# Kernel tuning notes

Hardware: AMD Instinct MI355X
Metric: run time of the kernel (lower is better)

Reference implementation:

```python
import jax, jax.numpy as jnp
import numpy as np

N_NODES = 100000
N_EDGES = 1600000
IN_FEATS = 128
HIDDEN = 128


def _graph_conv(x, W, b, src, dst, n_nodes):
    # DGL GraphConv with norm='both': out = D_in^{-1/2} * A^T * (D_out^{-1/2} * x) @ W + b
    ones = jnp.ones((src.shape[0],), dtype=x.dtype)
    deg_out = jax.ops.segment_sum(ones, src, num_segments=n_nodes)
    deg_in = jax.ops.segment_sum(ones, dst, num_segments=n_nodes)
    norm_src = jax.lax.rsqrt(jnp.clip(deg_out, 1.0))  # [N]
    norm_dst = jax.lax.rsqrt(jnp.clip(deg_in, 1.0))   # [N]
    h = x @ W                                          # [N, F_out]
    msg = h[src] * norm_src[src][:, None]              # gather by edge src: [E, F_out]
    agg = jax.ops.segment_sum(msg, dst, num_segments=n_nodes)  # scatter-add to dst
    return agg * norm_dst[:, None] + b


def setup_inputs() -> dict:
    key = jax.random.key(0)
    ks = jax.random.split(key, 9)
    x = jax.random.normal(ks[0], (N_NODES, IN_FEATS), dtype=jnp.float32)
    src = jax.random.randint(ks[1], (N_EDGES,), 0, N_NODES, dtype=jnp.int32)
    dst = jax.random.randint(ks[2], (N_EDGES,), 0, N_NODES, dtype=jnp.int32)
    s1 = 1.0 / np.sqrt(IN_FEATS)
    s2 = 1.0 / np.sqrt(HIDDEN)
    W1 = jax.random.uniform(ks[3], (IN_FEATS, HIDDEN), jnp.float32, -s1, s1)
    b1 = jnp.zeros((HIDDEN,), jnp.float32)
    W2 = jax.random.uniform(ks[4], (HIDDEN, HIDDEN), jnp.float32, -s2, s2)
    b2 = jnp.zeros((HIDDEN,), jnp.float32)
    sp = 1.0 / np.sqrt(2 * HIDDEN)
    Wp = jax.random.uniform(ks[5], (2 * HIDDEN, 1), jnp.float32, -sp, sp)
    bp = jax.random.uniform(ks[6], (1,), jnp.float32, -sp, sp)
    return {"x": x, "W1": W1, "b1": b1, "W2": W2, "b2": b2,
            "Wp": Wp, "bp": bp, "src": src, "dst": dst}


def reference(x, W1, b1, W2, b2, Wp, bp, src, dst):
    n_nodes = x.shape[0]
    h = _graph_conv(x, W1, b1, src, dst, n_nodes)
    h = jax.nn.relu(h)
    h = _graph_conv(h, W2, b2, src, dst, n_nodes)  # final node embeddings [N, H]
    # predict_links on the same edge list: cat(h[u], h[v]) -> linear -> sigmoid
    edge_h = jnp.concatenate([h[src], h[dst]], axis=1)  # [E, 2H]
    scores = jax.nn.sigmoid(edge_h @ Wp + bp)           # [E, 1]
    return scores
```

## Files before the change

### kernel.cpp

```cpp
#include <hip/hip_runtime.h>
#include <cstdint>
#include <cstddef>

#define NN 100000
#define NE 1600000
#define F  128
#define NPAD 100352
#define NBUCK 782
#define BCAPG 2560
#define FILLB 384
#define CHUNK 4167

typedef __attribute__((ext_vector_type(8))) short bf16x8;
typedef __attribute__((ext_vector_type(4))) float f32x4;

__device__ __forceinline__ unsigned short f2bf(float f) {
    unsigned u = __float_as_uint(f);
    unsigned r = (u + 0x7fffu + ((u >> 16) & 1u)) >> 16;
    return (unsigned short)r;
}
__device__ __forceinline__ void acc_bf8s(const uint4 v, const float ns, float* acc) {
    acc[0] += __uint_as_float(v.x << 16) * ns;
    acc[1] += __uint_as_float(v.x & 0xffff0000u) * ns;
    acc[2] += __uint_as_float(v.y << 16) * ns;
    acc[3] += __uint_as_float(v.y & 0xffff0000u) * ns;
    acc[4] += __uint_as_float(v.z << 16) * ns;
    acc[5] += __uint_as_float(v.z & 0xffff0000u) * ns;
    acc[6] += __uint_as_float(v.w << 16) * ns;
    acc[7] += __uint_as_float(v.w & 0xffff0000u) * ns;
}

__global__ void head_const_kernel(const float* __restrict__ b2, const float* __restrict__ Wp,
                                  const float* __restrict__ bp, float* __restrict__ consts) {
    const int l = threadIdx.x;
    const float2 bb = *(const float2*)&b2[2 * l];
    const float2 wa = *(const float2*)&Wp[2 * l];
    const float2 wc = *(const float2*)&Wp[F + 2 * l];
    float s = bb.x * (wa.x + wc.x) + bb.y * (wa.y + wc.y);
    #pragma unroll
    for (int m = 32; m > 0; m >>= 1) s += __shfl_xor(s, m);
    if (l == 0) consts[0] = s + bp[0];
}

__global__ void headw_kernel(const float* __restrict__ W2, const float* __restrict__ Wp,
                             float2* __restrict__ V) {
    const int i = threadIdx.x;
    float sa = 0.f, sc = 0.f;
    #pragma unroll 8
    for (int j = 0; j < F; ++j) {
        const float w = W2[i * F + j];
        sa += w * Wp[j];
        sc += w * Wp[F + j];
    }
    V[i] = make_float2(sa, sc);
}

__global__ void init_cursor_kernel(int* __restrict__ gCur) {
    const int b = blockIdx.x * blockDim.x + threadIdx.x;
    if (b < NBUCK) gCur[b] = b * BCAPG;
}

__global__ __launch_bounds__(256, 3)
void gemm1_fill_kernel(const float* __restrict__ in, const float* __restrict__ W,
                       unsigned short* __restrict__ out_bf,
                       const int* __restrict__ src, const int* __restrict__ dst,
                       int* __restrict__ deg_out, int* __restrict__ gCur,
                       int* __restrict__ srcPart) {
    __shared__ __align__(16) char smem[31264];

    const int g = blockIdx.x;
    const int tid = threadIdx.x;

    if (g & 1) {
        int* packedL = (int*)smem;
        unsigned short* bktL = (unsigned short*)(packedL + CHUNK);
        int* hist = (int*)((char*)smem + 25008);
        int* curL = hist + NBUCK;
        const int e0 = (g >> 1) * CHUNK;
        const int nCh = min(CHUNK, NE - e0);
        for (int i = tid; i < NBUCK; i += 256) hist[i] = 0;
        __syncthreads();
        for (int i = tid; i < nCh; i += 256) {
            const int s = src[e0 + i];
            const int d = dst[e0 + i];
            atomicAdd(&deg_out[s], 1);
            const int bkt = d >> 7;
            atomicAdd(&hist[bkt], 1);
            packedL[i] = s | ((d & 127) << 17);
            bktL[i] = (unsigned short)bkt;
        }
        __syncthreads();
        for (int b = tid; b < NBUCK; b += 256) {
            const int c = hist[b];
            curL[b] = (c > 0) ? atomicAdd(&gCur[b], c) : 0;
        }
        __syncthreads();
        for (int i = tid; i < nCh; i += 256) {
            const int bkt = bktL[i];
            const int p = atomicAdd(&curL[bkt], 1);
            if (p < (bkt + 1) * BCAPG)
                srcPart[p] = packedL[i];
        }
        return;
    }

    char* A_hi = smem;
    char* A_lo = smem + 8192;

    const int gid  = g >> 1;
    const int w    = tid >> 6;
    const int lane = tid & 63;
    const int ml   = lane & 15;
    const int quad = lane >> 4;

    bf16x8 Bf[4][2];
    #pragma unroll
    for (int kb = 0; kb < 4; ++kb) {
        #pragma unroll
        for (int nb = 0; nb < 2; ++nb) {
            const int n = 32 * w + nb * 16 + ml;
            const int k0 = kb * 32 + quad * 8;
            #pragma unroll
            for (int j = 0; j < 8; ++j)
                Bf[kb][nb][j] = (short)f2bf(W[(k0 + j) * F + n]);
        }
    }

    const int nTiles = NN / 32;
    for (int tile = gid; tile < nTiles; tile += 384) {
        const int row0 = tile * 32;
        __syncthreads();
        #pragma unroll
        for (int c = 0; c < 2; ++c) {
            const int i2 = tid + 256 * c;
            const int m  = i2 >> 4;
            const int o  = i2 & 15;
            const float* xr = &in[(size_t)(row0 + m) * F + o * 8];
            const float4 v0 = *(const float4*)xr;
            const float4 v1 = *(const float4*)(xr + 4);
            float xv[8] = {v0.x, v0.y, v0.z, v0.w, v1.x, v1.y, v1.z, v1.w};
            short hi8[8], lo8[8];
            #pragma unroll
            for (int j = 0; j < 8; ++j) {
                const unsigned short h = f2bf(xv[j]);
                hi8[j] = (short)h;
                lo8[j] = (short)f2bf(xv[j] - __uint_as_float((unsigned)h << 16));
            }
            const int kb2 = o >> 2, q2 = o & 3, ml2 = m & 15, mh2 = m >> 4;
            const int fo = (((mh2 * 4 + kb2) * 64) + q2 * 16 + ml2) * 16;
            *(bf16x8*)(A_hi + fo) = *(bf16x8*)hi8;
            *(bf16x8*)(A_lo + fo) = *(bf16x8*)lo8;
        }
        __syncthreads();

        f32x4 acc00 = {0,0,0,0}, acc01 = {0,0,0,0}, acc10 = {0,0,0,0}, acc11 = {0,0,0,0};
        #pragma unroll
        for (int kb = 0; kb < 4; ++kb) {
            const int o0 = (kb * 64 + lane) * 16;
            const int o1 = ((4 + kb) * 64 + lane) * 16;
            const bf16x8 ah0 = *(const bf16x8*)(A_hi + o0);
            const bf16x8 ah1 = *(const bf16x8*)(A_hi + o1);
            const bf16x8 al0 = *(const bf16x8*)(A_lo + o0);
            const bf16x8 al1 = *(const bf16x8*)(A_lo + o1);
            acc00 = __builtin_amdgcn_mfma_f32_16x16x32_bf16(ah0, Bf[kb][0], acc00, 0, 0, 0);
            acc00 = __builtin_amdgcn_mfma_f32_16x16x32_bf16(al0, Bf[kb][0], acc00, 0, 0, 0);
            acc01 = __builtin_amdgcn_mfma_f32_16x16x32_bf16(ah0, Bf[kb][1], acc01, 0, 0, 0);
            acc01 = __builtin_amdgcn_mfma_f32_16x16x32_bf16(al0, Bf[kb][1], acc01, 0, 0, 0);
            acc10 = __builtin_amdgcn_mfma_f32_16x16x32_bf16(ah1, Bf[kb][0], acc10, 0, 0, 0);
            acc10 = __builtin_amdgcn_mfma_f32_16x16x32_bf16(al1, Bf[kb][0], acc10, 0, 0, 0);
            acc11 = __builtin_amdgcn_mfma_f32_16x16x32_bf16(ah1, Bf[kb][1], acc11, 0, 0, 0);
            acc11 = __builtin_amdgcn_mfma_f32_16x16x32_bf16(al1, Bf[kb][1], acc11, 0, 0, 0);
        }

        #pragma unroll
        for (int mh = 0; mh < 2; ++mh) {
            #pragma unroll
            for (int nb = 0; nb < 2; ++nb) {
                const f32x4 a = (mh == 0) ? (nb == 0 ? acc00 : acc01)
                                          : (nb == 0 ? acc10 : acc11);
                const int row = row0 + mh * 16 + quad * 4;
                const int col = 32 * w + nb * 16 + ml;
                #pragma unroll
                for (int r = 0; r < 4; ++r)
                    out_bf[(size_t)(row + r) * F + col] = f2bf(a[r]);
            }
        }
    }
}

__global__ void normsrc_kernel(const int* __restrict__ deg_out, float* __restrict__ norm_src, int nN) {
    const int n = blockIdx.x * blockDim.x + threadIdx.x;
    if (n < nN) norm_src[n] = rsqrtf((float)max(deg_out[n], 1));
}

__global__ __launch_bounds__(256)
void gather_sort_kernel(const unsigned short* __restrict__ hs,
                        int* __restrict__ srcPart, const int* __restrict__ gCur,
                        const float* __restrict__ norm_src, const float* __restrict__ bias,
                        const float2* __restrict__ V, float2* __restrict__ uw,
                        int* __restrict__ offs, int* __restrict__ ends,
                        float* __restrict__ norm_dst) {
    __shared__ int cnt[128];
    __shared__ int loc[128];
    __shared__ int cur[128];
    __shared__ int sortedL[BCAPG];

    const int b   = blockIdx.x;
    const int tid = threadIdx.x;
    const int nlo = b * 128;
    const int nCnt = min(128, NN - nlo);
    const int eBase = b * BCAPG;
    const int total = min(gCur[b] - eBase, BCAPG);

    if (tid < 128) cnt[tid] = 0;
    __syncthreads();
    for (int i = tid; i < total; i += 256)
        atomicAdd(&cnt[(srcPart[eBase + i] >> 17) & 127], 1);
    __syncthreads();
    if (tid < 128) loc[tid] = cnt[tid];
    __syncthreads();
    for (int off = 1; off < 128; off <<= 1) {
        int v = 0;
        if (tid < 128 && tid >= off) v = loc[tid - off];
        __syncthreads();
        if (tid < 128) loc[tid] += v;
        __syncthreads();
    }
    if (tid < 128) cur[tid] = loc[tid] - cnt[tid];
    if (tid < nCnt) {
        const int st = eBase + loc[tid] - cnt[tid];
        offs[nlo + tid] = st;
        ends[nlo + tid] = st + cnt[tid];
        norm_dst[nlo + tid] = rsqrtf((float)max(cnt[tid], 1));
    }
    __syncthreads();
    for (int i = tid; i < total; i += 256) {
        const int v = srcPart[eBase + i];
        const int r = atomicAdd(&cur[(v >> 17) & 127], 1);
        sortedL[r] = v & 0x1FFFF;
    }
    __syncthreads();
    for (int i = tid; i < total; i += 256)
        srcPart[eBase + i] = sortedL[i];

    const int w  = tid >> 6;
    const int l  = tid & 63;
    const int q  = l >> 4;
    const int c8 = (l & 15) * 8;
    float bb[8];
    *(float4*)&bb[0] = *(const float4*)&bias[c8];
    *(float4*)&bb[4] = *(const float4*)&bias[c8 + 4];
    float2 Vl[8];
    #pragma unroll
    for (int k = 0; k < 8; ++k) Vl[k] = V[c8 + k];

    const int nhEnd = min((w + 1) * 32, nCnt);
    for (int nh = w * 32; nh < nhEnd; ++nh) {
        const int end = loc[nh];
        const int beg = end - cnt[nh];
        float acc[8] = {0.f, 0.f, 0.f, 0.f, 0.f, 0.f, 0.f, 0.f};
        int j = beg;
        for (; j + 16 <= end; j += 16) {
            const int s0 = sortedL[j + q];
            const int s1 = sortedL[j + 4 + q];
            const int s2 = sortedL[j + 8 + q];
            const int s3 = sortedL[j + 12 + q];
            const float ns0 = norm_src[s0];
            const float ns1 = norm_src[s1];
            const float ns2 = norm_src[s2];
            const float ns3 = norm_src[s3];
            const uint4 v0 = *(const uint4*)&hs[(size_t)s0 * F + c8];
            const uint4 v1 = *(const uint4*)&hs[(size_t)s1 * F + c8];
            const uint4 v2 = *(const uint4*)&hs[(size_t)s2 * F + c8];
            const uint4 v3 = *(const uint4*)&hs[(size_t)s3 * F + c8];
            acc_bf8s(v0, ns0, acc);
            acc_bf8s(v1, ns1, acc);
            acc_bf8s(v2, ns2, acc);
            acc_bf8s(v3, ns3, acc);
        }
        for (; j + 8 <= end; j += 8) {
            const int s0 = sortedL[j + q];
            const int s1 = sortedL[j + 4 + q];
            const float ns0 = norm_src[s0];
            const float ns1 = norm_src[s1];
            const uint4 v0 = *(const uint4*)&hs[(size_t)s0 * F + c8];
            const uint4 v1 = *(const uint4*)&hs[(size_t)s1 * F + c8];
            acc_bf8s(v0, ns0, acc);
            acc_bf8s(v1, ns1, acc);
        }
        for (; j + 4 <= end; j += 4) {
            const int s = sortedL[j + q];
            const float ns = norm_src[s];
            const uint4 v = *(const uint4*)&hs[(size_t)s * F + c8];
            acc_bf8s(v, ns, acc);
        }
        if (j + q < end) {
            const int s = sortedL[j + q];
            const float ns = norm_src[s];
            const uint4 v = *(const uint4*)&hs[(size_t)s * F + c8];
            acc_bf8s(v, ns, acc);
        }
        #pragma unroll
        for (int k = 0; k < 8; ++k) {
            acc[k] += __shfl_xor(acc[k], 16);
            acc[k] += __shfl_xor(acc[k], 32);
        }

        const int n = nlo + nh;
        const float nd = rsqrtf((float)max(cnt[nh], 1));
        float pa = 0.f, pc = 0.f;
        #pragma unroll
        for (int k = 0; k < 8; ++k) {
            const float ok = fmaxf(acc[k] * nd + bb[k], 0.f);
            pa += ok * Vl[k].x;
            pc += ok * Vl[k].y;
        }
        #pragma unroll
        for (int m = 1; m <= 8; m <<= 1) {
            pa += __shfl_xor(pa, m);
            pc += __shfl_xor(pc, m);
        }
        if (l == 0) {
            const float ns = norm_src[n];
            uw[n] = make_float2(ns * pa, ns * pc);
        }
    }
}

__global__ void ac_kernel(const float2* __restrict__ uw, const int* __restrict__ sorted_src,
                          const int* __restrict__ offs, const int* __restrict__ ends,
                          const float* __restrict__ norm_dst,
                          float* __restrict__ A, float* __restrict__ C, int nN) {
    const int n = blockIdx.x * blockDim.x + threadIdx.x;
    if (n >= nN) return;
    const int beg = offs[n];
    const int end = ends[n];
    float su = 0.f, sw = 0.f;
    int j = beg;
    for (; j + 2 <= end; j += 2) {
        const float2 t0 = uw[sorted_src[j]];
        const float2 t1 = uw[sorted_src[j + 1]];
        su += t0.x + t1.x;
        sw += t0.y + t1.y;
    }
    if (j < end) {
        const float2 t = uw[sorted_src[j]];
        su += t.x;
        sw += t.y;
    }
    const float nd = norm_dst[n];
    A[n] = nd * su;
    C[n] = nd * sw;
}

__global__ void score_kernel(const float* __restrict__ A, const float* __restrict__ C,
                             const int* __restrict__ src, const int* __restrict__ dst,
                             const float* __restrict__ consts, float* __restrict__ out, int nE) {
    const int e = blockIdx.x * blockDim.x + threadIdx.x;
    if (e < nE) {
        const float z = A[src[e]] + C[dst[e]] + consts[0];
        out[e] = 1.f / (1.f + __expf(-z));
    }
}

extern "C" void kernel_launch(void* const* d_in, const int* in_sizes, int n_in,
                              void* d_out, int out_size, void* d_ws, size_t ws_size,
                              hipStream_t stream) {
    const float* x  = (const float*)d_in[0];
    const float* W1 = (const float*)d_in[1];
    const float* b1 = (const float*)d_in[2];
    const float* W2 = (const float*)d_in[3];
    const float* b2 = (const float*)d_in[4];
    const float* Wp = (const float*)d_in[5];
    const float* bp = (const float*)d_in[6];
    const int*   src = (const int*)d_in[7];
    const int*   dst = (const int*)d_in[8];
    float* out = (float*)d_out;

    float* ws        = (float*)d_ws;
    float* norm_src  = ws;
    float* bufA      = ws + NPAD;
    float* bufC      = ws + 2 * NPAD;
    float* norm_dst  = ws + 3 * NPAD;
    int*   offs      = (int*)(ws + 4 * NPAD);
    int*   ends      = offs + NPAD;
    int*   gCur      = ends + NPAD;
    float* consts    = (float*)(gCur + 1024);
    float2* V        = (float2*)(consts + 16);
    float2* uw       = V + 128;
    int*   srcPart   = (int*)(uw + NN);
    unsigned short* hs_bf = (unsigned short*)(srcPart + NBUCK * BCAPG);

    hipMemsetAsync(bufA, 0, NPAD * sizeof(int), stream);
    init_cursor_kernel<<<4, 256, 0, stream>>>(gCur);
    head_const_kernel<<<1, 64, 0, stream>>>(b2, Wp, bp, consts);
    headw_kernel<<<1, 128, 0, stream>>>(W2, Wp, V);

    gemm1_fill_kernel<<<768, 256, 0, stream>>>(x, W1, hs_bf, src, dst,
                                               (int*)bufA, gCur, srcPart);

    normsrc_kernel<<<(NN + 255) / 256, 256, 0, stream>>>((const int*)bufA, norm_src, NN);

    gather_sort_kernel<<<NBUCK, 256, 0, stream>>>(hs_bf, srcPart, gCur, norm_src, b1,
                                                  V, uw, offs, ends, norm_dst);

    ac_kernel<<<(NN + 255) / 256, 256, 0, stream>>>(uw, srcPart, offs, ends, norm_dst,
                                                    bufA, bufC, NN);

    score_kernel<<<(NE + 255) / 256, 256, 0, stream>>>(bufA, bufC, src, dst, consts, out, NE);
}
```

Baseline: 314.8 us.

## Split hidden features into column quarters and gather per quarter to improve cache reuse

The GEMM now writes the bf16 hidden matrix as four column-quarter planes of 32 features each. A separate gather kernel runs one pass per quarter, and a combine kernel sums the four partial head projections. The sort kernel writes sorted indices to a new buffer, and extra blocks pre-scale the hidden rows by norm_src in place so the gather skips the per-edge norm load. Each quarter plane is about 6.4MB, which should fit better in cache during the random gathers. The cost is more kernel launches, an extra read-modify-write pass over the hidden matrix, a second bf16 rounding after scaling, and re-reading the sorted indices four times.

```diff
diff --git a/kernel.cpp b/kernel.cpp
--- a/kernel.cpp
+++ b/kernel.cpp
@@ -8,8 +8,8 @@
 #define NPAD 100352
 #define NBUCK 782
 #define BCAPG 2560
-#define FILLB 384
 #define CHUNK 4167
+#define SCALEB 512
 
 typedef __attribute__((ext_vector_type(8))) short bf16x8;
 typedef __attribute__((ext_vector_type(4))) float f32x4;
@@ -19,15 +19,16 @@
     unsigned r = (u + 0x7fffu + ((u >> 16) & 1u)) >> 16;
     return (unsigned short)r;
 }
-__device__ __forceinline__ void acc_bf8s(const uint4 v, const float ns, float* acc) {
-    acc[0] += __uint_as_float(v.x << 16) * ns;
-    acc[1] += __uint_as_float(v.x & 0xffff0000u) * ns;
-    acc[2] += __uint_as_float(v.y << 16) * ns;
-    acc[3] += __uint_as_float(v.y & 0xffff0000u) * ns;
-    acc[4] += __uint_as_float(v.z << 16) * ns;
-    acc[5] += __uint_as_float(v.z & 0xffff0000u) * ns;
-    acc[6] += __uint_as_float(v.w << 16) * ns;
-    acc[7] += __uint_as_float(v.w & 0xffff0000u) * ns;
+__device__ __forceinline__ void acc_bf4(const uint2 v, float* acc) {
+    acc[0] += __uint_as_float(v.x << 16);
+    acc[1] += __uint_as_float(v.x & 0xffff0000u);
+    acc[2] += __uint_as_float(v.y << 16);
+    acc[3] += __uint_as_float(v.y & 0xffff0000u);
+}
+__device__ __forceinline__ unsigned scale2bf(unsigned p, float ns) {
+    const float a = __uint_as_float(p << 16) * ns;
+    const float b = __uint_as_float(p & 0xffff0000u) * ns;
+    return (unsigned)f2bf(a) | ((unsigned)f2bf(b) << 16);
 }
 
 __global__ void head_const_kernel(const float* __restrict__ b2, const float* __restrict__ Wp,
@@ -125,6 +126,8 @@
                 Bf[kb][nb][j] = (short)f2bf(W[(k0 + j) * F + n]);
         }
     }
+
+    unsigned short* outq = out_bf + (size_t)w * NN * 32;
 
     const int nTiles = NN / 32;
     for (int tile = gid; tile < nTiles; tile += 384) {
@@ -179,10 +182,10 @@
                 const f32x4 a = (mh == 0) ? (nb == 0 ? acc00 : acc01)
                                           : (nb == 0 ? acc10 : acc11);
                 const int row = row0 + mh * 16 + quad * 4;
-                const int col = 32 * w + nb * 16 + ml;
+                const int sc  = nb * 16 + ml;
                 #pragma unroll
                 for (int r = 0; r < 4; ++r)
-                    out_bf[(size_t)(row + r) * F + col] = f2bf(a[r]);
+                    outq[(size_t)(row + r) * 32 + sc] = f2bf(a[r]);
             }
         }
     }
@@ -194,19 +197,37 @@
 }
 
 __global__ __launch_bounds__(256)
-void gather_sort_kernel(const unsigned short* __restrict__ hs,
-                        int* __restrict__ srcPart, const int* __restrict__ gCur,
-                        const float* __restrict__ norm_src, const float* __restrict__ bias,
-                        const float2* __restrict__ V, float2* __restrict__ uw,
-                        int* __restrict__ offs, int* __restrict__ ends,
-                        float* __restrict__ norm_dst) {
+void sortscale_kernel(const int* __restrict__ srcPart, const int* __restrict__ gCur,
+                      int* __restrict__ sortedOut, const float* __restrict__ norm_src,
+                      unsigned short* __restrict__ hs,
+                      int* __restrict__ offs, int* __restrict__ ends,
+                      float* __restrict__ norm_dst) {
     __shared__ int cnt[128];
     __shared__ int loc[128];
     __shared__ int cur[128];
     __shared__ int sortedL[BCAPG];
 
-    const int b   = blockIdx.x;
+    const int g = blockIdx.x;
     const int tid = threadIdx.x;
+
+    if (g >= NBUCK) {
+        const int sb = g - NBUCK;
+        uint4* hs4 = (uint4*)hs;
+        const int total4 = NN * 16;
+        for (int i = sb * 256 + tid; i < total4; i += SCALEB * 256) {
+            const int node = (i >> 2) % NN;
+            const float ns = norm_src[node];
+            uint4 v = hs4[i];
+            v.x = scale2bf(v.x, ns);
+            v.y = scale2bf(v.y, ns);
+            v.z = scale2bf(v.z, ns);
+            v.w = scale2bf(v.w, ns);
+            hs4[i] = v;
+        }
+        return;
+    }
+
+    const int b   = g;
     const int nlo = b * 128;
     const int nCnt = min(128, NN - nlo);
     const int eBase = b * BCAPG;
@@ -241,89 +262,91 @@
     }
     __syncthreads();
     for (int i = tid; i < total; i += 256)
-        srcPart[eBase + i] = sortedL[i];
-
-    const int w  = tid >> 6;
-    const int l  = tid & 63;
-    const int q  = l >> 4;
-    const int c8 = (l & 15) * 8;
-    float bb[8];
-    *(float4*)&bb[0] = *(const float4*)&bias[c8];
-    *(float4*)&bb[4] = *(const float4*)&bias[c8 + 4];
-    float2 Vl[8];
+        sortedOut[eBase + i] = sortedL[i];
+}
+
+__global__ __launch_bounds__(256)
+void gather4_kernel(const unsigned short* __restrict__ hs, const int* __restrict__ sortedOut,
+                    const int* __restrict__ offs, const int* __restrict__ ends,
+                    const float* __restrict__ norm_dst, const float* __restrict__ norm_src,
+                    const float* __restrict__ b1, const float2* __restrict__ V,
+                    float2* __restrict__ uwQ) {
+    const int blk = blockIdx.x;
+    const int ph  = blk / NBUCK;
+    const int b   = blk - ph * NBUCK;
+    const int tid = threadIdx.x;
+    const int w   = tid >> 6;
+    const int l   = tid & 63;
+    const int eo  = l >> 3;
+    const int cl  = l & 7;
+    const int nlo = b * 128;
+    const int nCnt = min(128, NN - nlo);
+    const unsigned short* hsq = hs + (size_t)ph * NN * 32;
+
+    const int kb = ph * 32 + cl * 4;
+    float bb[4];
+    *(float4*)bb = *(const float4*)&b1[kb];
+    float2 Vl[4];
     #pragma unroll
-    for (int k = 0; k < 8; ++k) Vl[k] = V[c8 + k];
+    for (int k = 0; k < 4; ++k) Vl[k] = V[kb + k];
 
     const int nhEnd = min((w + 1) * 32, nCnt);
     for (int nh = w * 32; nh < nhEnd; ++nh) {
-        const int end = loc[nh];
-        const int beg = end - cnt[nh];
-        float acc[8] = {0.f, 0.f, 0.f, 0.f, 0.f, 0.f, 0.f, 0.f};
+        const int n = nlo + nh;
+        const int beg = offs[n];
+        const int end = ends[n];
+        float acc[4] = {0.f, 0.f, 0.f, 0.f};
         int j = beg;
         for (; j + 16 <= end; j += 16) {
-            const int s0 = sortedL[j + q];
-            const int s1 = sortedL[j + 4 + q];
-            const int s2 = sortedL[j + 8 + q];
-            const int s3 = sortedL[j + 12 + q];
-            const float ns0 = norm_src[s0];
-            const float ns1 = norm_src[s1];
-            const float ns2 = norm_src[s2];
-            const float ns3 = norm_src[s3];
-            const uint4 v0 = *(const uint4*)&hs[(size_t)s0 * F + c8];
-            const uint4 v1 = *(const uint4*)&hs[(size_t)s1 * F + c8];
-            const uint4 v2 = *(const uint4*)&hs[(size_t)s2 * F + c8];
-            const uint4 v3 = *(const uint4*)&hs[(size_t)s3 * F + c8];
-            acc_bf8s(v0, ns0, acc);
-            acc_bf8s(v1, ns1, acc);
-            acc_bf8s(v2, ns2, acc);
-            acc_bf8s(v3, ns3, acc);
+            const int s0 = sortedOut[j + eo];
+            const int s1 = sortedOut[j + 8 + eo];
+            const uint2 v0 = *(const uint2*)&hsq[(size_t)s0 * 32 + cl * 4];
+            const uint2 v1 = *(const uint2*)&hsq[(size_t)s1 * 32 + cl * 4];
+            acc_bf4(v0, acc);
+            acc_bf4(v1, acc);
         }
         for (; j + 8 <= end; j += 8) {
-            const int s0 = sortedL[j + q];
-            const int s1 = sortedL[j + 4 + q];
-            const float ns0 = norm_src[s0];
-            const float ns1 = norm_src[s1];
-            const uint4 v0 = *(const uint4*)&hs[(size_t)s0 * F + c8];
-            const uint4 v1 = *(const uint4*)&hs[(size_t)s1 * F + c8];
-            acc_bf8s(v0, ns0, acc);
-            acc_bf8s(v1, ns1, acc);
-        }
-        for (; j + 4 <= end; j += 4) {
-            const int s = sortedL[j + q];
-            const float ns = norm_src[s];
-            const uint4 v = *(const uint4*)&hs[(size_t)s * F + c8];
-            acc_bf8s(v, ns, acc);
-        }
-        if (j + q < end) {
-            const int s = sortedL[j + q];
-            const float ns = norm_src[s];
-            const uint4 v = *(const uint4*)&hs[(size_t)s * F + c8];
-            acc_bf8s(v, ns, acc);
-        }
-        #pragma unroll
-        for (int k = 0; k < 8; ++k) {
+            const int s = sortedOut[j + eo];
+            acc_bf4(*(const uint2*)&hsq[(size_t)s * 32 + cl * 4], acc);
+        }
+        if (j + eo < end) {
+            const int s = sortedOut[j + eo];
+            acc_bf4(*(const uint2*)&hsq[(size_t)s * 32 + cl * 4], acc);
+        }
+        #pragma unroll
+        for (int k = 0; k < 4; ++k) {
+            acc[k] += __shfl_xor(acc[k], 8);
             acc[k] += __shfl_xor(acc[k], 16);
             acc[k] += __shfl_xor(acc[k], 32);
         }
-
-        const int n = nlo + nh;
-        const float nd = rsqrtf((float)max(cnt[nh], 1));
+        const float nd = norm_dst[n];
         float pa = 0.f, pc = 0.f;
         #pragma unroll
-        for (int k = 0; k < 8; ++k) {
+        for (int k = 0; k < 4; ++k) {
             const float ok = fmaxf(acc[k] * nd + bb[k], 0.f);
             pa += ok * Vl[k].x;
             pc += ok * Vl[k].y;
         }
         #pragma unroll
-        for (int m = 1; m <= 8; m <<= 1) {
+        for (int m = 1; m <= 4; m <<= 1) {
             pa += __shfl_xor(pa, m);
             pc += __shfl_xor(pc, m);
         }
         if (l == 0) {
             const float ns = norm_src[n];
-            uw[n] = make_float2(ns * pa, ns * pc);
-        }
+            uwQ[(size_t)ph * NN + n] = make_float2(ns * pa, ns * pc);
+        }
+    }
+}
+
+__global__ void combine_kernel(const float2* __restrict__ uwQ, float2* __restrict__ uw, int nN) {
+    const int n = blockIdx.x * blockDim.x + threadIdx.x;
+    if (n < nN) {
+        const float2 a = uwQ[n];
+        const float2 b = uwQ[NN + n];
+        const float2 c = uwQ[2 * NN + n];
+        const float2 d = uwQ[3 * NN + n];
+        uw[n] = make_float2(a.x + b.x + c.x + d.x, a.y + b.y + c.y + d.y);
     }
 }
 
@@ -388,8 +411,10 @@
     float* consts    = (float*)(gCur + 1024);
     float2* V        = (float2*)(consts + 16);
     float2* uw       = V + 128;
-    int*   srcPart   = (int*)(uw + NN);
-    unsigned short* hs_bf = (unsigned short*)(srcPart + NBUCK * BCAPG);
+    float2* uwQ      = uw + NN;
+    int*   srcPart   = (int*)(uwQ + 4 * NN);
+    int*   sortedOut = srcPart + (size_t)NBUCK * BCAPG;
+    unsigned short* hs_bf = (unsigned short*)(sortedOut + (size_t)NBUCK * BCAPG);
 
     hipMemsetAsync(bufA, 0, NPAD * sizeof(int), stream);
     init_cursor_kernel<<<4, 256, 0, stream>>>(gCur);
@@ -401,10 +426,16 @@
 
     normsrc_kernel<<<(NN + 255) / 256, 256, 0, stream>>>((const int*)bufA, norm_src, NN);
 
-    gather_sort_kernel<<<NBUCK, 256, 0, stream>>>(hs_bf, srcPart, gCur, norm_src, b1,
-                                                  V, uw, offs, ends, norm_dst);
-
-    ac_kernel<<<(NN + 255) / 256, 256, 0, stream>>>(uw, srcPart, offs, ends, norm_dst,
+    sortscale_kernel<<<NBUCK + SCALEB, 256, 0, stream>>>(srcPart, gCur, sortedOut,
+                                                         norm_src, hs_bf,
+                                                         offs, ends, norm_dst);
+
+    gather4_kernel<<<NBUCK * 4, 256, 0, stream>>>(hs_bf, sortedOut, offs, ends,
+                                                  norm_dst, norm_src, b1, V, uwQ);
+
+    combine_kernel<<<(NN + 255) / 256, 256, 0, stream>>>(uwQ, uw, NN);
+
+    ac_kernel<<<(NN + 255) / 256, 256, 0, stream>>>(uw, sortedOut, offs, ends, norm_dst,
                                                     bufA, bufC, NN);
 
     score_kernel<<<(NE + 255) / 256, 256, 0, stream>>>(bufA, bufC, src, dst, consts, out, NE);
```

Measured after the change: 400.9 us. 27.3% more time.
